# Optimization experiments

Hardware: AMD Instinct MI355X
Metric: run time of the kernel (lower is better)

Reference implementation:

```python
import jax, jax.numpy as jnp
import numpy as np

N_LAYERS = 3
HEADS = 2
HID = 64
IN_DIM = 10
NEG_SLOPE = 0.2  # DGL EGATConv leaky_relu default
B, NPG = 8, 6250  # batch_size, nodes per graph (== max_n_nodes)
N = B * NPG
E = 500000
N_RES = 30  # max_n_resources


def _mlp2(x, W0, b0, W1, b1):
    return jax.nn.relu(x @ W0 + b0) @ W1 + b1


def _segment_softmax(e, dst, n):
    # softmax over incoming edges of each destination node (DGL edge_softmax)
    m = jax.ops.segment_max(e, dst, num_segments=n)
    m = jnp.where(jnp.isfinite(m), m, 0.0)
    ex = jnp.exp(e - m[dst])
    s = jax.ops.segment_sum(ex, dst, num_segments=n)
    return ex / (s[dst] + 1e-9)


def _egat(h, f, src, dst, W_ni, W_nj, W_fij, W_node, attn, bias):
    # per-edge attention features: f_ni[src] + f_nj[dst] + f_fij + bias
    f_out = (h @ W_ni)[src] + (h @ W_nj)[dst] + f @ W_fij + bias   # (E, H*HID)
    f_out = jax.nn.leaky_relu(f_out, NEG_SLOPE).reshape(-1, HEADS, HID)
    e = (f_out * attn[None]).sum(-1)                               # (E, H)
    alpha = _segment_softmax(e, dst, h.shape[0])
    msg = alpha[:, :, None] * (h @ W_node).reshape(-1, HEADS, HID)[src]
    h_out = jax.ops.segment_sum(msg, dst, num_segments=h.shape[0])  # (N, H, HID)
    return h_out, f_out


def _forward(feat, att_rc, att_rp, etype_emb, rid_emb, rc_W, rc_b, rp_W, rp_b,
             fe_W0, fe_b0, fe_W1, fe_b1,
             W_ni, W_nj, W_fij, W_node, attn, egat_bias,
             Wm0, bm0, Wm1, bm1, src, dst, etype, rid):
    feats_list = [feat]
    h = _mlp2(feat, fe_W0, fe_b0, fe_W1, fe_b1)
    feats_list.append(h)
    # 'sum' edge embedding flavor
    emb = etype_emb[etype] + rid_emb[rid] + (att_rc @ rc_W + rc_b) + (att_rp @ rp_W + rp_b)
    for l in range(N_LAYERS):
        h_att, _ = _egat(h, emb, src, dst, W_ni[l], W_nj[l], W_fij[l], W_node[l],
                         attn[l], egat_bias[l])
        h = _mlp2(h_att.reshape(-1, HEADS * HID), Wm0[l], bm0[l], Wm1[l], bm1[l]) + feats_list[-1]
        feats_list.append(h)
    features = jnp.concatenate(feats_list, axis=1)       # (N, IN_DIM + HID*(L+1))
    node_features = features.reshape(B, NPG, -1)
    graph_embedding = node_features.max(axis=1)          # graph_pooling='max'
    rep = jnp.broadcast_to(graph_embedding[:, None, :], node_features.shape)
    return jnp.concatenate([node_features, rep], axis=2)  # (B, NPG, 2*F)


def setup_inputs():
    key = jax.random.key(0)
    ks = iter(jax.random.split(key, 40))
    def rn(shape, s=0.1):
        return jax.random.normal(next(ks), shape, dtype=jnp.float32) * s
    HO = HEADS * HID
    inp = {}
    inp['feat'] = rn((N, IN_DIM), 1.0)
    inp['att_rc'] = rn((E, 2), 1.0)
    inp['att_rp'] = rn((E, 3), 1.0)
    inp['etype_emb'] = rn((7, HID))
    inp['rid_emb'] = rn((N_RES + 1, HID))
    inp['rc_W'] = rn((2, HID)); inp['rc_b'] = rn((HID,))
    inp['rp_W'] = rn((3, HID)); inp['rp_b'] = rn((HID,))
    inp['fe_W0'] = rn((IN_DIM, HID)); inp['fe_b0'] = rn((HID,))
    inp['fe_W1'] = rn((HID, HID)); inp['fe_b1'] = rn((HID,))
    inp['W_ni'] = rn((N_LAYERS, HID, HO)); inp['W_nj'] = rn((N_LAYERS, HID, HO))
    inp['W_fij'] = rn((N_LAYERS, HID, HO)); inp['W_node'] = rn((N_LAYERS, HID, HO))
    inp['attn'] = rn((N_LAYERS, HEADS, HID)); inp['egat_bias'] = rn((N_LAYERS, HO))
    inp['Wm0'] = rn((N_LAYERS, HO, HO)); inp['bm0'] = rn((N_LAYERS, HO))
    inp['Wm1'] = rn((N_LAYERS, HO, HID)); inp['bm1'] = rn((N_LAYERS, HID))
    inp['src'] = jax.random.randint(next(ks), (E,), 0, N, dtype=jnp.int32)
    inp['dst'] = jax.random.randint(next(ks), (E,), 0, N, dtype=jnp.int32)
    inp['etype'] = jax.random.randint(next(ks), (E,), 0, 7, dtype=jnp.int32)
    inp['rid'] = jax.random.randint(next(ks), (E,), 0, N_RES + 1, dtype=jnp.int32)
    return inp


def reference(feat, att_rc, att_rp, etype_emb, rid_emb, rc_W, rc_b, rp_W, rp_b,
              fe_W0, fe_b0, fe_W1, fe_b1, W_ni, W_nj, W_fij, W_node, attn, egat_bias,
              Wm0, bm0, Wm1, bm1, src, dst, etype, rid):
    return _forward(feat, att_rc, att_rp, etype_emb, rid_emb, rc_W, rc_b, rp_W, rp_b,
                    fe_W0, fe_b0, fe_W1, fe_b1, W_ni, W_nj, W_fij, W_node, attn, egat_bias,
                    Wm0, bm0, Wm1, bm1, src, dst, etype, rid)
```

## Files before the change

kernel.cpp:

```cpp
#include <hip/hip_runtime.h>
#include <hip/hip_bf16.h>
#include <math.h>

#define N_NODES 50000
#define N_EDGES 500000
#define B_GRAPHS 8
#define NPG 6250
#define HID 64
#define HO 128
#define IN_DIM 10
#define F_TOT 266
#define OUT_C 532
#define NEG_SLOPE 0.2f
#define NT_ROWS 44
#define SCB 200
#define SCH 250

typedef short bf16x8 __attribute__((ext_vector_type(8)));
typedef float f32x4 __attribute__((ext_vector_type(4)));
typedef float f32x2 __attribute__((ext_vector_type(2)));
typedef unsigned u32x2v __attribute__((ext_vector_type(2)));

__device__ __forceinline__ float LD(const void* p, size_t i, int f32) {
    if (f32) return ((const float*)p)[i];
    unsigned u = ((const unsigned short*)p)[i];
    return __uint_as_float(u << 16);
}
__device__ __forceinline__ unsigned fkey(float f) {
    unsigned b = __float_as_uint(f);
    return (b & 0x80000000u) ? ~b : (b | 0x80000000u);
}
__device__ __forceinline__ float funkey(unsigned k) {
    unsigned b = (k & 0x80000000u) ? (k & 0x7fffffffu) : ~k;
    return __uint_as_float(b);
}
__device__ __forceinline__ unsigned short rnebf(float x) {
    unsigned u = __float_as_uint(x);
    return (unsigned short)((u + 0x7FFFu + ((u >> 16) & 1u)) >> 16);
}
__device__ __forceinline__ unsigned pk2(float lo, float hi) {
    return (unsigned)rnebf(lo) | ((unsigned)rnebf(hi) << 16);
}
__device__ __forceinline__ float plo(unsigned u) { return __uint_as_float(u << 16); }
__device__ __forceinline__ float phi(unsigned u) { return __uint_as_float(u & 0xFFFF0000u); }
__device__ __forceinline__ f32x2 up2(unsigned u) {
    return (f32x2){__uint_as_float(u << 16), __uint_as_float(u & 0xFFFF0000u)};
}
__device__ __forceinline__ void pswap(float& a, float& b) {
    u32x2v r = __builtin_amdgcn_permlane32_swap(__float_as_uint(a), __float_as_uint(b),
                                                false, false);
    a = __uint_as_float(r.x);
    b = __uint_as_float(r.y);
}

__global__ void k_detect(const void* __restrict__ att_rc, int* __restrict__ flagp) {
    __shared__ int cnt;
    if (threadIdx.x == 0) cnt = 0;
    __syncthreads();
    const unsigned short* w = (const unsigned short*)att_rc;
    int c = 0;
    for (int i = threadIdx.x; i < 8192; i += 256) {
        unsigned e = (w[i] >> 7) & 0xFF;
        if (e >= 0xC0) c++;
    }
    atomicAdd(&cnt, c);
    __syncthreads();
    if (threadIdx.x == 0) *flagp = (cnt > 8) ? 1 : 0;
}

__global__ void k_wprep(const void* __restrict__ W_ni, const void* __restrict__ W_nj,
                        const void* __restrict__ W_node, const void* __restrict__ Wm0,
                        const void* __restrict__ Wm1,
                        unsigned short* __restrict__ pw_n,
                        unsigned short* __restrict__ pw_m0,
                        unsigned short* __restrict__ pw_m1,
                        const int* __restrict__ flagp) {
    const int f32 = *flagp;
    int i = blockIdx.x * 256 + threadIdx.x;
    if (i < 73728) {
        int k = i & 63, c = (i >> 6) & 127, lm = i >> 13;
        int m = lm % 3, l = lm / 3;
        const void* W = (m == 0) ? W_ni : (m == 1) ? W_nj : W_node;
        pw_n[i] = rnebf(LD(W, (size_t)l * 8192 + k * 128 + c, f32));
    } else if (i < 73728 + 49152) {
        int j = i - 73728;
        int k = j & 127, c = (j >> 7) & 127, l = j >> 14;
        pw_m0[j] = rnebf(LD(Wm0, (size_t)l * 16384 + k * 128 + c, f32));
    } else if (i < 147456) {
        int j = i - 122880;
        int k = j & 127, c = (j >> 7) & 63, l = j >> 13;
        pw_m1[j] = rnebf(LD(Wm1, (size_t)l * 8192 + k * 64 + c, f32));
    }
}

__global__ void k_count(const int* __restrict__ dst, int* __restrict__ cnt) {
    int i = blockIdx.x * blockDim.x + threadIdx.x;
    int stride = gridDim.x * blockDim.x;
    for (int e = i; e < N_EDGES; e += stride) atomicAdd(&cnt[dst[e]], 1);
}

__global__ void k_scan1(const int* __restrict__ cnt, int* __restrict__ bsum) {
    __shared__ int red[256];
    int b = blockIdx.x, t = threadIdx.x;
    red[t] = (t < SCH) ? cnt[b * SCH + t] : 0;
    __syncthreads();
    for (int off = 128; off; off >>= 1) {
        if (t < off) red[t] += red[t + off];
        __syncthreads();
    }
    if (t == 0) bsum[b] = red[0];
}
__global__ void k_scan2(const int* __restrict__ bsum, int* __restrict__ boff) {
    __shared__ int ts[256];
    int t = threadIdx.x;
    int v = (t < SCB) ? bsum[t] : 0;
    ts[t] = v;
    __syncthreads();
    for (int off = 1; off < 256; off <<= 1) {
        int u = (t >= off) ? ts[t - off] : 0;
        __syncthreads();
        ts[t] += u;
        __syncthreads();
    }
    if (t < SCB) boff[t] = ts[t] - v;
}
__global__ void k_scan3(const int* __restrict__ cnt, const int* __restrict__ boff,
                        int* __restrict__ rowptr, int* __restrict__ cursor) {
    __shared__ int ts[256];
    int b = blockIdx.x, t = threadIdx.x;
    int base = b * SCH;
    int v = (t < SCH) ? cnt[base + t] : 0;
    ts[t] = v;
    __syncthreads();
    for (int off = 1; off < 256; off <<= 1) {
        int u = (t >= off) ? ts[t - off] : 0;
        __syncthreads();
        ts[t] += u;
        __syncthreads();
    }
    if (t < SCH) {
        int r = boff[b] + ts[t] - v;
        rowptr[base + t] = r;
        cursor[base + t] = r;
    }
    if (b == SCB - 1 && t == SCH - 1) rowptr[N_NODES] = boff[b] + ts[t];
}

__global__ void k_fill(const int* __restrict__ src, const int* __restrict__ dst,
                       const int* __restrict__ etype, const int* __restrict__ rid,
                       const void* __restrict__ att_rc, const void* __restrict__ att_rp,
                       int* __restrict__ cursor, uint4* __restrict__ emeta,
                       const int* __restrict__ flagp) {
    const int f32 = *flagp;
    int i = blockIdx.x * blockDim.x + threadIdx.x;
    int stride = gridDim.x * blockDim.x;
    for (int e = i; e < N_EDGES; e += stride) {
        int d = dst[e];
        int j = atomicAdd(&cursor[d], 1);
        float rc0 = LD(att_rc, 2 * (size_t)e, f32), rc1 = LD(att_rc, 2 * (size_t)e + 1, f32);
        float rp0 = LD(att_rp, 3 * (size_t)e, f32), rp1 = LD(att_rp, 3 * (size_t)e + 1, f32),
              rp2 = LD(att_rp, 3 * (size_t)e + 2, f32);
        uint4 m;
        m.x = pk2(rc0, rc1);
        m.y = pk2(rp0, rp1);
        m.z = pk2(rp2, 0.f);
        m.w = (unsigned)(etype[e] | (rid[e] << 3) | ((unsigned)src[e] << 8));
        emeta[j] = m;
    }
}

__global__ void k_init(const void* __restrict__ feat,
                       const void* __restrict__ W0, const void* __restrict__ b0,
                       const void* __restrict__ W1, const void* __restrict__ b1,
                       float* __restrict__ feats, const int* __restrict__ flagp) {
    const int f32 = *flagp;
    __shared__ float sf[64 * 12];
    __shared__ float sW0[IN_DIM * 64];
    __shared__ float sb0[64], sb1[64];
    __shared__ float sh[64 * 64];
    __shared__ float sW1[64 * 64];
    int tid = threadIdx.x, n0 = blockIdx.x * 64;
    for (int i = tid; i < IN_DIM * 64; i += 256) sW0[i] = LD(W0, i, f32);
    for (int i = tid; i < 64; i += 256) { sb0[i] = LD(b0, i, f32); sb1[i] = LD(b1, i, f32); }
    for (int i = tid; i < 64 * 64; i += 256) sW1[i] = LD(W1, i, f32);
    for (int i = tid; i < 64 * IN_DIM; i += 256) {
        int n = n0 + i / IN_DIM, c = i % IN_DIM;
        sf[(i / IN_DIM) * 12 + c] = (n < N_NODES) ? LD(feat, (size_t)n * IN_DIM + c, f32) : 0.f;
    }
    __syncthreads();
    int ng = tid / 16, cg = tid % 16;
    float acc[4][4];
    #pragma unroll
    for (int i = 0; i < 4; i++)
        #pragma unroll
        for (int j = 0; j < 4; j++) acc[i][j] = sb0[cg * 4 + j];
    #pragma unroll
    for (int k = 0; k < IN_DIM; k++)
        #pragma unroll
        for (int i = 0; i < 4; i++) {
            float a = sf[(ng * 4 + i) * 12 + k];
            #pragma unroll
            for (int j = 0; j < 4; j++) acc[i][j] += a * sW0[k * 64 + cg * 4 + j];
        }
    #pragma unroll
    for (int i = 0; i < 4; i++)
        #pragma unroll
        for (int j = 0; j < 4; j++) sh[(ng * 4 + i) * 64 + cg * 4 + j] = fmaxf(acc[i][j], 0.f);
    __syncthreads();
    float o[4][4];
    #pragma unroll
    for (int i = 0; i < 4; i++)
        #pragma unroll
        for (int j = 0; j < 4; j++) o[i][j] = sb1[cg * 4 + j];
    for (int k = 0; k < 64; k++) {
        float4 bv = *(const float4*)&sW1[k * 64 + cg * 4];
        #pragma unroll
        for (int i = 0; i < 4; i++) {
            float a = sh[(ng * 4 + i) * 64 + k];
            o[i][0] += a * bv.x; o[i][1] += a * bv.y;
            o[i][2] += a * bv.z; o[i][3] += a * bv.w;
        }
    }
    #pragma unroll
    for (int i = 0; i < 4; i++) {
        int n = n0 + ng * 4 + i;
        if (n < N_NODES) {
            float* r = feats + (size_t)n * F_TOT;
            #pragma unroll
            for (int j = 0; j < 4; j++) r[IN_DIM + cg * 4 + j] = o[i][j];
        }
    }
    for (int i = tid; i < 64 * IN_DIM; i += 256) {
        int n = n0 + i / IN_DIM, c = i % IN_DIM;
        if (n < N_NODES) feats[(size_t)n * F_TOT + c] = sf[(i / IN_DIM) * 12 + c];
    }
}

__global__ void k_tables(const void* __restrict__ etype_emb, const void* __restrict__ rid_emb,
                         const void* __restrict__ rc_W, const void* __restrict__ rc_b,
                         const void* __restrict__ rp_W, const void* __restrict__ rp_b,
                         const void* __restrict__ W_fij, const void* __restrict__ egat_bias,
                         float* __restrict__ T, const int* __restrict__ flagp) {
    const int f32 = *flagp;
    int l = blockIdx.x;
    __shared__ float S[NT_ROWS * HID];
    __shared__ float W[HID * HO];
    for (int i = threadIdx.x; i < 7 * HID; i += 256) S[i] = LD(etype_emb, i, f32);
    for (int i = threadIdx.x; i < 31 * HID; i += 256) S[7 * HID + i] = LD(rid_emb, i, f32);
    for (int i = threadIdx.x; i < 2 * HID; i += 256) S[38 * HID + i] = LD(rc_W, i, f32);
    for (int i = threadIdx.x; i < 3 * HID; i += 256) S[40 * HID + i] = LD(rp_W, i, f32);
    for (int i = threadIdx.x; i < HID; i += 256)
        S[43 * HID + i] = LD(rc_b, i, f32) + LD(rp_b, i, f32);
    for (int i = threadIdx.x; i < HID * HO; i += 256)
        W[i] = LD(W_fij, (size_t)l * HID * HO + i, f32);
    __syncthreads();
    for (int idx = threadIdx.x; idx < NT_ROWS * HO; idx += 256) {
        int r = idx / HO, c = idx % HO;
        float acc = (r == 43) ? LD(egat_bias, l * HO + c, f32) : 0.f;
        for (int k = 0; k < HID; k++) acc += S[r * HID + k] * W[k * HO + c];
        T[(size_t)l * NT_ROWS * HO + idx] = acc;
    }
}

__global__ void __launch_bounds__(256) k_ngemm(
        const float* __restrict__ feats, int h_off,
        const unsigned short* __restrict__ pw_n, int l,
        unsigned* __restrict__ gsrc, unsigned* __restrict__ gdst) {
    __shared__ __align__(16) unsigned short Xs[64 * 72];
    __shared__ __align__(16) unsigned short Ws[384 * 72];
    int tid = threadIdx.x, n0 = blockIdx.x * 64;
    for (int i = tid; i < 64 * 64; i += 256) {
        int n = i >> 6, c = i & 63, gn = n0 + n;
        Xs[n * 72 + c] = rnebf((gn < N_NODES) ? feats[(size_t)gn * F_TOT + h_off + c] : 0.f);
    }
    const uint4* pn = (const uint4*)pw_n + (size_t)l * 3072;
    for (int i = tid; i < 3072; i += 256) {
        int kq = i & 7, mc = i >> 3;
        *(uint4*)&Ws[mc * 72 + kq * 8] = pn[i];
    }
    __syncthreads();
    int wid = tid >> 6, lane = tid & 63;
    int row0 = wid * 16, mrow = lane & 15, quad = lane >> 4;
    bf16x8 a0 = *(const bf16x8*)&Xs[(row0 + mrow) * 72 + quad * 8];
    bf16x8 a1 = *(const bf16x8*)&Xs[(row0 + mrow) * 72 + 32 + quad * 8];
    f32x4 accA[8], accB[8];
    #pragma unroll
    for (int j = 0; j < 8; j++) { accA[j] = (f32x4){0,0,0,0}; accB[j] = (f32x4){0,0,0,0}; }
    #pragma unroll
    for (int j = 0; j < 8; j++) {
        bf16x8 b0 = *(const bf16x8*)&Ws[(0 * 128 + j * 16 + mrow) * 72 + quad * 8];
        bf16x8 b1 = *(const bf16x8*)&Ws[(0 * 128 + j * 16 + mrow) * 72 + 32 + quad * 8];
        accA[j] = __builtin_amdgcn_mfma_f32_16x16x32_bf16(a0, b0, accA[j], 0, 0, 0);
        accA[j] = __builtin_amdgcn_mfma_f32_16x16x32_bf16(a1, b1, accA[j], 0, 0, 0);
        bf16x8 c0 = *(const bf16x8*)&Ws[(2 * 128 + j * 16 + mrow) * 72 + quad * 8];
        bf16x8 c1 = *(const bf16x8*)&Ws[(2 * 128 + j * 16 + mrow) * 72 + 32 + quad * 8];
        accB[j] = __builtin_amdgcn_mfma_f32_16x16x32_bf16(a0, c0, accB[j], 0, 0, 0);
        accB[j] = __builtin_amdgcn_mfma_f32_16x16x32_bf16(a1, c1, accB[j], 0, 0, 0);
    }
    #pragma unroll
    for (int j = 0; j < 4; j++) {
        int c = j * 16 + mrow;
        #pragma unroll
        for (int r = 0; r < 4; r++) {
            int gn = n0 + row0 + quad * 4 + r;
            if (gn < N_NODES) {
                uint2 v;
                v.x = pk2(accA[j][r], accA[j + 4][r]);
                v.y = pk2(accB[j][r], accB[j + 4][r]);
                *(uint2*)&gsrc[(size_t)gn * 128 + c * 2] = v;
            }
        }
    }
    f32x4 accC[8];
    #pragma unroll
    for (int j = 0; j < 8; j++) accC[j] = (f32x4){0,0,0,0};
    #pragma unroll
    for (int j = 0; j < 8; j++) {
        bf16x8 b0 = *(const bf16x8*)&Ws[(1 * 128 + j * 16 + mrow) * 72 + quad * 8];
        bf16x8 b1 = *(const bf16x8*)&Ws[(1 * 128 + j * 16 + mrow) * 72 + 32 + quad * 8];
        accC[j] = __builtin_amdgcn_mfma_f32_16x16x32_bf16(a0, b0, accC[j], 0, 0, 0);
        accC[j] = __builtin_amdgcn_mfma_f32_16x16x32_bf16(a1, b1, accC[j], 0, 0, 0);
    }
    #pragma unroll
    for (int j = 0; j < 4; j++) {
        int c = j * 16 + mrow;
        #pragma unroll
        for (int r = 0; r < 4; r++) {
            int gn = n0 + row0 + quad * 4 + r;
            if (gn < N_NODES)
                gdst[(size_t)gn * 64 + c] = pk2(accC[j][r], accC[j + 4][r]);
        }
    }
}

__global__ void __launch_bounds__(256) k_edge_fused(
        const float* __restrict__ T, const void* __restrict__ attn, int l,
        const unsigned* __restrict__ gsrc, const unsigned* __restrict__ gdst,
        const int* __restrict__ rowptr, const uint4* __restrict__ emeta,
        float* __restrict__ h_att, const int* __restrict__ flagp) {
    const int f32 = *flagp;
    __shared__ f32x2 Ts2[38 * 64];
    const float* Tl = T + (size_t)l * NT_ROWS * HO;
    int tid = threadIdx.x;
    for (int i = tid; i < 38 * 64; i += 256) {
        int r = i >> 6, c = i & 63;
        Ts2[i] = (f32x2){Tl[r * HO + c], Tl[r * HO + 64 + c]};
    }
    int lane = tid & 63;
    f32x2 C2[6];
    #pragma unroll
    for (int r = 0; r < 6; r++)
        C2[r] = (f32x2){Tl[(38 + r) * HO + lane], Tl[(38 + r) * HO + 64 + lane]};
    f32x2 AT2 = (f32x2){LD(attn, l * HO + lane, f32), LD(attn, l * HO + 64 + lane, f32)};
    __syncthreads();
    int wid = tid >> 6;
    int d0 = blockIdx.x * 8 + wid * 2;

    #pragma unroll 1
    for (int dn = 0; dn < 2; dn++) {
        int d = d0 + dn;
        int jb = rowptr[d], je = rowptr[d + 1];
        int last = je - 1;
        if (last < jb) last = jb;
        if (last > N_EDGES - 1) last = N_EDGES - 1;
        unsigned gd = gdst[(size_t)d * 64 + lane];
        f32x2 NJ2 = up2(gd) + C2[5];
        f32x2 A2 = (f32x2){0.f, 0.f};
        float Lsp = 0.f;

        auto logits = [&](const uint4& em, const uint2& g, float& s_out, f32x2& h2) {
            unsigned w = em.w;
            int et = (int)(w & 7u), ri = (int)((w >> 3) & 31u);
            f32x2 x = up2(g.x) + NJ2;
            x += Ts2[et * 64 + lane];
            x += Ts2[(7 + ri) * 64 + lane];
            x += plo(em.x) * C2[0];
            x += phi(em.x) * C2[1];
            x += plo(em.y) * C2[2];
            x += phi(em.y) * C2[3];
            x += plo(em.z) * C2[4];
            f32x2 xs = x * NEG_SLOPE;
            x.x = fmaxf(x.x, xs.x);
            x.y = fmaxf(x.y, xs.y);
            f32x2 p = x * AT2;
            h2 = up2(g.y);
            float pa = p.x, pb = p.y;
            pswap(pa, pb);
            float s = pa + pb;
            s += __int_as_float(__builtin_amdgcn_update_dpp(0, __float_as_int(s), 0xB1, 0xF, 0xF, true));
            s += __int_as_float(__builtin_amdgcn_update_dpp(0, __float_as_int(s), 0x4E, 0xF, 0xF, true));
            s += __int_as_float(__builtin_amdgcn_update_dpp(0, __float_as_int(s), 0x141, 0xF, 0xF, true));
            s += __int_as_float(__builtin_amdgcn_update_dpp(0, __float_as_int(s), 0x140, 0xF, 0xF, true));
            s += __int_as_float(__builtin_amdgcn_ds_swizzle(__float_as_int(s), 0x401F));
            s_out = s;
        };
        auto update = [&](float w, f32x2 h2) {
            Lsp += w;
            float wa = w, wb = w;
            pswap(wa, wb);
            A2 += (f32x2){wa, wb} * h2;
        };
        auto fetch = [&](int j_, uint4& em, uint2& g) {
            int jj = (j_ < last) ? j_ : last;
            em = emeta[jj];
            g = *(const uint2*)&gsrc[(size_t)(em.w >> 8) * 128 + lane * 2];
        };

        uint4 emA, emB, emC, emD;
        uint2 gA, gB, gC, gD;
        fetch(jb,     emA, gA);
        fetch(jb + 1, emB, gB);
        fetch(jb + 2, emC, gC);
        fetch(jb + 3, emD, gD);
        #pragma unroll 1
        for (int j = jb; j < je; j += 4) {
            float sA, sB, sC, sD;
            f32x2 hA, hB, hC, hD;
            logits(emA, gA, sA, hA);
            logits(emB, gB, sB, hB);
            logits(emC, gC, sC, hC);
            logits(emD, gD, sD, hD);
            float wA = __expf(sA);
            float wB = (j + 1 < je) ? __expf(sB) : 0.f;
            float wC = (j + 2 < je) ? __expf(sC) : 0.f;
            float wD = (j + 3 < je) ? __expf(sD) : 0.f;
            if (j + 4 < je) {
                fetch(j + 4, emA, gA);
                fetch(j + 5, emB, gB);
                fetch(j + 6, emC, gC);
                fetch(j + 7, emD, gD);
            }
            update(wA, hA);
            update(wB, hB);
            update(wC, hC);
            update(wD, hD);
        }

        float la = Lsp, lb = Lsp;
        pswap(la, lb);
        h_att[(size_t)d * HO + lane]      = A2.x / (la + 1e-9f);
        h_att[(size_t)d * HO + 64 + lane] = A2.y / (lb + 1e-9f);
    }
}

__global__ void __launch_bounds__(256) k_mlp(
        const float* __restrict__ h_att,
        const unsigned short* __restrict__ pw_m0, const void* __restrict__ bm0,
        const unsigned short* __restrict__ pw_m1, const void* __restrict__ bm1, int l,
        float* __restrict__ feats, int prev_off, int out_off,
        const int* __restrict__ flagp) {
    const int f32 = *flagp;
    __shared__ __align__(16) unsigned short Xs[64 * 136];
    __shared__ __align__(16) unsigned short W0T[128 * 136];
    __shared__ __align__(16) unsigned short W1T[64 * 136];
    __shared__ float sb0[HO], sb1[64];
    int tid = threadIdx.x, n0 = blockIdx.x * 64;
    for (int i = tid; i < 64 * 128; i += 256) {
        int n = i >> 7, c = i & 127, gn = n0 + n;
        Xs[n * 136 + c] = rnebf((gn < N_NODES) ? h_att[(size_t)gn * HO + c] : 0.f);
    }
    const uint4* p0 = (const uint4*)pw_m0 + (size_t)l * 2048;
    for (int i = tid; i < 2048; i += 256) {
        int kq = i & 15, c = i >> 4;
        *(uint4*)&W0T[c * 136 + kq * 8] = p0[i];
    }
    const uint4* p1 = (const uint4*)pw_m1 + (size_t)l * 1024;
    for (int i = tid; i < 1024; i += 256) {
        int kq = i & 15, c = i >> 4;
        *(uint4*)&W1T[c * 136 + kq * 8] = p1[i];
    }
    for (int i = tid; i < HO; i += 256) sb0[i] = LD(bm0, l * HO + i, f32);
    for (int i = tid; i < 64; i += 256) sb1[i] = LD(bm1, l * 64 + i, f32);
    __syncthreads();
    int wid = tid >> 6, lane = tid & 63;
    int row0 = wid * 16, mrow = lane & 15, quad = lane >> 4;
    f32x4 acc[8];
    #pragma unroll
    for (int j = 0; j < 8; j++) {
        float b = sb0[j * 16 + mrow];
        acc[j] = (f32x4){b, b, b, b};
    }
    #pragma unroll
    for (int ks = 0; ks < 4; ks++) {
        bf16x8 a = *(const bf16x8*)&Xs[(row0 + mrow) * 136 + ks * 32 + quad * 8];
        #pragma unroll
        for (int j = 0; j < 8; j++) {
            bf16x8 b = *(const bf16x8*)&W0T[(j * 16 + mrow) * 136 + ks * 32 + quad * 8];
            acc[j] = __builtin_amdgcn_mfma_f32_16x16x32_bf16(a, b, acc[j], 0, 0, 0);
        }
    }
    #pragma unroll
    for (int j = 0; j < 8; j++)
        #pragma unroll
        for (int r = 0; r < 4; r++)
            Xs[(row0 + quad * 4 + r) * 136 + j * 16 + mrow] = rnebf(fmaxf(acc[j][r], 0.f));
    f32x4 o[4];
    #pragma unroll
    for (int j = 0; j < 4; j++) {
        float b = sb1[j * 16 + mrow];
        o[j] = (f32x4){b, b, b, b};
    }
    #pragma unroll
    for (int ks = 0; ks < 4; ks++) {
        bf16x8 a = *(const bf16x8*)&Xs[(row0 + mrow) * 136 + ks * 32 + quad * 8];
        #pragma unroll
        for (int j = 0; j < 4; j++) {
            bf16x8 b = *(const bf16x8*)&W1T[(j * 16 + mrow) * 136 + ks * 32 + quad * 8];
            o[j] = __builtin_amdgcn_mfma_f32_16x16x32_bf16(a, b, o[j], 0, 0, 0);
        }
    }
    #pragma unroll
    for (int j = 0; j < 4; j++) {
        int c = j * 16 + mrow;
        #pragma unroll
        for (int r = 0; r < 4; r++) {
            int gn = n0 + row0 + quad * 4 + r;
            if (gn < N_NODES) {
                float* rw = feats + (size_t)gn * F_TOT;
                rw[out_off + c] = o[j][r] + rw[prev_off + c];
            }
        }
    }
}

__global__ void k_pool(const float* __restrict__ feats, unsigned* __restrict__ gmax) {
    int g = blockIdx.x;
    int chunk = blockIdx.y;
    int t = threadIdx.x;
    const int CS = 49;
    int nb = chunk * CS;
    int ne = (nb + CS < NPG) ? nb + CS : NPG;
    float m0 = -INFINITY, m1 = -INFINITY;
    for (int n = nb; n < ne; n++) {
        const float* row = feats + (size_t)(g * NPG + n) * F_TOT;
        m0 = fmaxf(m0, row[t]);
        if (t + 256 < F_TOT) m1 = fmaxf(m1, row[t + 256]);
    }
    atomicMax(&gmax[g * F_TOT + t], fkey(m0));
    if (t + 256 < F_TOT) atomicMax(&gmax[g * F_TOT + t + 256], fkey(m1));
}

__global__ void k_out(const float* __restrict__ feats, const unsigned* __restrict__ gmax,
                      void* __restrict__ out, const int* __restrict__ flagp) {
    const int f32 = *flagp;
    int lane = threadIdx.x & 63;
    int wave = (blockIdx.x * blockDim.x + threadIdx.x) >> 6;
    int nw = (gridDim.x * blockDim.x) >> 6;
    for (int row = wave; row < B_GRAPHS * NPG; row += nw) {
        int g = row / NPG;
        const float* fr = feats + (size_t)row * F_TOT;
        const unsigned* gr = gmax + g * F_TOT;
        if (f32) {
            float* o = (float*)out + (size_t)row * OUT_C;
            for (int c = lane; c < OUT_C; c += 64)
                o[c] = (c < F_TOT) ? fr[c] : funkey(gr[c - F_TOT]);
        } else {
            __hip_bfloat16* o = (__hip_bfloat16*)out + (size_t)row * OUT_C;
            for (int c = lane; c < OUT_C; c += 64)
                o[c] = __float2bfloat16((c < F_TOT) ? fr[c] : funkey(gr[c - F_TOT]));
        }
    }
}

extern "C" void kernel_launch(void* const* d_in, const int* in_sizes, int n_in,
                              void* d_out, int out_size, void* d_ws, size_t ws_size,
                              hipStream_t stream) {
    const void* feat      = d_in[0];
    const void* att_rc    = d_in[1];
    const void* att_rp    = d_in[2];
    const void* etype_emb = d_in[3];
    const void* rid_emb   = d_in[4];
    const void* rc_W      = d_in[5];
    const void* rc_b      = d_in[6];
    const void* rp_W      = d_in[7];
    const void* rp_b      = d_in[8];
    const void* fe_W0     = d_in[9];
    const void* fe_b0     = d_in[10];
    const void* fe_W1     = d_in[11];
    const void* fe_b1     = d_in[12];
    const void* W_ni      = d_in[13];
    const void* W_nj      = d_in[14];
    const void* W_fij     = d_in[15];
    const void* W_node    = d_in[16];
    const void* attn      = d_in[17];
    const void* egat_bias = d_in[18];
    const void* Wm0       = d_in[19];
    const void* bm0       = d_in[20];
    const void* Wm1       = d_in[21];
    const void* bm1       = d_in[22];
    const int* src   = (const int*)d_in[23];
    const int* dst   = (const int*)d_in[24];
    const int* etype = (const int*)d_in[25];
    const int* rid   = (const int*)d_in[26];

    char* p = (char*)d_ws;
    auto alloc = [&](size_t bytes) {
        char* r = p;
        p += (bytes + 255) & ~(size_t)255;
        return r;
    };
    float*    feats  = (float*)alloc((size_t)N_NODES * F_TOT * 4);
    unsigned* gsrc   = (unsigned*)alloc((size_t)N_NODES * HO * 4);
    unsigned* gdst   = (unsigned*)alloc((size_t)N_NODES * 64 * 4);
    float*    h_att  = (float*)alloc((size_t)N_NODES * HO * 4);
    float*    T      = (float*)alloc((size_t)3 * NT_ROWS * HO * 4);
    unsigned* gmax   = (unsigned*)alloc((size_t)B_GRAPHS * F_TOT * 4);
    int*      flagp  = (int*)alloc(256);
    int*      rowptr = (int*)alloc((size_t)(N_NODES + 1) * 4);
    int*      cursor = (int*)alloc((size_t)N_NODES * 4);
    int*      cnt    = (int*)alloc((size_t)N_NODES * 4);
    int*      bsum   = (int*)alloc((size_t)SCB * 4);
    int*      boff   = (int*)alloc((size_t)SCB * 4);
    uint4*    emeta  = (uint4*)alloc((size_t)N_EDGES * 16);
    unsigned short* pw_n  = (unsigned short*)alloc((size_t)73728 * 2);
    unsigned short* pw_m0 = (unsigned short*)alloc((size_t)49152 * 2);
    unsigned short* pw_m1 = (unsigned short*)alloc((size_t)24576 * 2);

    k_detect<<<1, 256, 0, stream>>>(att_rc, flagp);
    hipMemsetAsync(cnt, 0, (size_t)N_NODES * 4, stream);
    hipMemsetAsync(gmax, 0, (size_t)B_GRAPHS * F_TOT * 4, stream);
    k_wprep<<<576, 256, 0, stream>>>(W_ni, W_nj, W_node, Wm0, Wm1,
                                     pw_n, pw_m0, pw_m1, flagp);
    k_count<<<512, 256, 0, stream>>>(dst, cnt);
    k_scan1<<<SCB, 256, 0, stream>>>(cnt, bsum);
    k_scan2<<<1, 256, 0, stream>>>(bsum, boff);
    k_scan3<<<SCB, 256, 0, stream>>>(cnt, boff, rowptr, cursor);
    k_fill<<<1024, 256, 0, stream>>>(src, dst, etype, rid, att_rc, att_rp,
                                     cursor, emeta, flagp);
    k_init<<<(N_NODES + 63) / 64, 256, 0, stream>>>(feat, fe_W0, fe_b0, fe_W1, fe_b1,
                                                    feats, flagp);
    k_tables<<<3, 256, 0, stream>>>(etype_emb, rid_emb, rc_W, rc_b, rp_W, rp_b,
                                    W_fij, egat_bias, T, flagp);
    for (int l = 0; l < 3; l++) {
        int h_off = IN_DIM + l * HID;
        int out_off = IN_DIM + (l + 1) * HID;
        k_ngemm<<<(N_NODES + 63) / 64, 256, 0, stream>>>(feats, h_off, pw_n, l, gsrc, gdst);
        k_edge_fused<<<N_NODES / 8, 256, 0, stream>>>(T, attn, l, gsrc, gdst,
                                                      rowptr, emeta, h_att, flagp);
        k_mlp<<<(N_NODES + 63) / 64, 256, 0, stream>>>(h_att, pw_m0, bm0, pw_m1, bm1, l,
                                                       feats, h_off, out_off, flagp);
    }
    k_pool<<<dim3(B_GRAPHS, 128), 256, 0, stream>>>(feats, gmax);
    k_out<<<2048, 256, 0, stream>>>(feats, gmax, d_out, flagp);
}
```

Before: 755.4 us.

## Deepen edge-loop prefetch pipeline with two-stage metadata/gather staging and scalarized indices

```diff
diff --git a/kernel.cpp b/kernel.cpp
--- a/kernel.cpp
+++ b/kernel.cpp
@@ -351,7 +351,9 @@
     #pragma unroll
     for (int r = 0; r < 6; r++)
         C2[r] = (f32x2){Tl[(38 + r) * HO + lane], Tl[(38 + r) * HO + 64 + lane]};
-    f32x2 AT2 = (f32x2){LD(attn, l * HO + lane, f32), LD(attn, l * HO + 64 + lane, f32)};
+    const float LOG2E = 1.4426950408889634f;
+    f32x2 AT2 = (f32x2){LD(attn, l * HO + lane, f32) * LOG2E,
+                        LD(attn, l * HO + 64 + lane, f32) * LOG2E};
     __syncthreads();
     int wid = tid >> 6;
     int d0 = blockIdx.x * 8 + wid * 2;
@@ -359,7 +361,8 @@
     #pragma unroll 1
     for (int dn = 0; dn < 2; dn++) {
         int d = d0 + dn;
-        int jb = rowptr[d], je = rowptr[d + 1];
+        int jb = __builtin_amdgcn_readfirstlane(rowptr[d]);
+        int je = __builtin_amdgcn_readfirstlane(rowptr[d + 1]);
         int last = je - 1;
         if (last < jb) last = jb;
         if (last > N_EDGES - 1) last = N_EDGES - 1;
@@ -368,9 +371,16 @@
         f32x2 A2 = (f32x2){0.f, 0.f};
         float Lsp = 0.f;
 
+        auto fe = [&](int j_) -> uint4 {
+            int jj = (j_ < last) ? j_ : last;
+            jj = __builtin_amdgcn_readfirstlane(jj);
+            return emeta[jj];
+        };
+        auto fg = [&](const uint4& em) -> uint2 {
+            return *(const uint2*)&gsrc[(size_t)(em.w >> 8) * 128 + lane * 2];
+        };
         auto logits = [&](const uint4& em, const uint2& g, float& s_out, f32x2& h2) {
-            unsigned w = em.w;
-            int et = (int)(w & 7u), ri = (int)((w >> 3) & 31u);
+            int et = (int)(em.w & 7u), ri = (int)((em.w >> 3) & 31u);
             f32x2 x = up2(g.x) + NJ2;
             x += Ts2[et * 64 + lane];
             x += Ts2[(7 + ri) * 64 + lane];
@@ -380,8 +390,7 @@
             x += phi(em.y) * C2[3];
             x += plo(em.z) * C2[4];
             f32x2 xs = x * NEG_SLOPE;
-            x.x = fmaxf(x.x, xs.x);
-            x.y = fmaxf(x.y, xs.y);
+            x = __builtin_elementwise_max(x, xs);
             f32x2 p = x * AT2;
             h2 = up2(g.y);
             float pa = p.x, pb = p.y;
@@ -394,46 +403,54 @@
             s += __int_as_float(__builtin_amdgcn_ds_swizzle(__float_as_int(s), 0x401F));
             s_out = s;
         };
-        auto update = [&](float w, f32x2 h2) {
+        auto upd = [&](float w, f32x2 h2) {
             Lsp += w;
             float wa = w, wb = w;
             pswap(wa, wb);
             A2 += (f32x2){wa, wb} * h2;
         };
-        auto fetch = [&](int j_, uint4& em, uint2& g) {
-            int jj = (j_ < last) ? j_ : last;
-            em = emeta[jj];
-            g = *(const uint2*)&gsrc[(size_t)(em.w >> 8) * 128 + lane * 2];
-        };
-
-        uint4 emA, emB, emC, emD;
-        uint2 gA, gB, gC, gD;
-        fetch(jb,     emA, gA);
-        fetch(jb + 1, emB, gB);
-        fetch(jb + 2, emC, gC);
-        fetch(jb + 3, emD, gD);
+
+        uint4 eA0 = fe(jb),     eA1 = fe(jb + 1), eA2 = fe(jb + 2), eA3 = fe(jb + 3);
+        uint4 eB0 = fe(jb + 4), eB1 = fe(jb + 5), eB2 = fe(jb + 6), eB3 = fe(jb + 7);
+        uint2 gA0 = fg(eA0), gA1 = fg(eA1), gA2 = fg(eA2), gA3 = fg(eA3);
+        int j = jb;
         #pragma unroll 1
-        for (int j = jb; j < je; j += 4) {
-            float sA, sB, sC, sD;
-            f32x2 hA, hB, hC, hD;
-            logits(emA, gA, sA, hA);
-            logits(emB, gB, sB, hB);
-            logits(emC, gC, sC, hC);
-            logits(emD, gD, sD, hD);
-            float wA = __expf(sA);
-            float wB = (j + 1 < je) ? __expf(sB) : 0.f;
-            float wC = (j + 2 < je) ? __expf(sC) : 0.f;
-            float wD = (j + 3 < je) ? __expf(sD) : 0.f;
-            if (j + 4 < je) {
-                fetch(j + 4, emA, gA);
-                fetch(j + 5, emB, gB);
-                fetch(j + 6, emC, gC);
-                fetch(j + 7, emD, gD);
+        while (j < je) {
+            uint4 eC0 = fe(j + 8), eC1 = fe(j + 9), eC2 = fe(j + 10), eC3 = fe(j + 11);
+            uint2 gB0 = fg(eB0), gB1 = fg(eB1), gB2 = fg(eB2), gB3 = fg(eB3);
+            {
+                float s0, s1, s2, s3;
+                f32x2 h0, h1, h2v, h3;
+                logits(eA0, gA0, s0, h0);
+                logits(eA1, gA1, s1, h1);
+                logits(eA2, gA2, s2, h2v);
+                logits(eA3, gA3, s3, h3);
+                float w0 = __builtin_exp2f(s0);
+                float w1 = (j + 1 < je) ? __builtin_exp2f(s1) : 0.f;
+                float w2 = (j + 2 < je) ? __builtin_exp2f(s2) : 0.f;
+                float w3 = (j + 3 < je) ? __builtin_exp2f(s3) : 0.f;
+                upd(w0, h0); upd(w1, h1); upd(w2, h2v); upd(w3, h3);
             }
-            update(wA, hA);
-            update(wB, hB);
-            update(wC, hC);
-            update(wD, hD);
+            if (j + 4 >= je) break;
+            uint4 eD0 = fe(j + 12), eD1 = fe(j + 13), eD2 = fe(j + 14), eD3 = fe(j + 15);
+            uint2 gN0 = fg(eC0), gN1 = fg(eC1), gN2 = fg(eC2), gN3 = fg(eC3);
+            {
+                float s0, s1, s2, s3;
+                f32x2 h0, h1, h2v, h3;
+                logits(eB0, gB0, s0, h0);
+                logits(eB1, gB1, s1, h1);
+                logits(eB2, gB2, s2, h2v);
+                logits(eB3, gB3, s3, h3);
+                float w0 = __builtin_exp2f(s0);
+                float w1 = (j + 5 < je) ? __builtin_exp2f(s1) : 0.f;
+                float w2 = (j + 6 < je) ? __builtin_exp2f(s2) : 0.f;
+                float w3 = (j + 7 < je) ? __builtin_exp2f(s3) : 0.f;
+                upd(w0, h0); upd(w1, h1); upd(w2, h2v); upd(w3, h3);
+            }
+            eA0 = eC0; eA1 = eC1; eA2 = eC2; eA3 = eC3;
+            eB0 = eD0; eB1 = eD1; eB2 = eD2; eB3 = eD3;
+            gA0 = gN0; gA1 = gN1; gA2 = gN2; gA3 = gN3;
+            j += 8;
         }
 
         float la = Lsp, lb = Lsp;
```

After: 720.1 us. 1.05x faster.
